# Kernel tuning notes

Hardware: AMD Instinct MI355X
Metric: run time of the kernel (lower is better)

## Reference

```python
import jax, jax.numpy as jnp
import numpy as np

B, S, D = 4, 2048, 1152
H, KVH, HD = 16, 4, 64
SW = 1792
NEG = jnp.float32(-1e9)


def setup_inputs() -> dict:
    key = jax.random.key(0)
    ks = jax.random.split(key, 6)
    x = jax.random.normal(ks[0], (B, S, D), jnp.float32)
    s = 0.02
    wq = jax.random.normal(ks[1], (H * HD, D), jnp.float32) * s
    wk = jax.random.normal(ks[2], (KVH * HD, D), jnp.float32) * s
    wv = jax.random.normal(ks[3], (KVH * HD, D), jnp.float32) * s
    wo = jax.random.normal(ks[4], (D, H * HD), jnp.float32) * s
    # rotary freqs: theta=10000, standard llama-style
    inv = 1.0 / (10000.0 ** (np.arange(0, HD, 2, dtype=np.float32) / HD))
    t = np.arange(S, dtype=np.float32)
    fr = np.outer(t, inv)  # [S, HD//2]
    freqs_cos = jnp.asarray(np.cos(fr), jnp.float32)
    freqs_sin = jnp.asarray(np.sin(fr), jnp.float32)
    positions = jnp.arange(S, dtype=jnp.int32)
    # sliding-window causal additive mask: attend j iff 0 <= i-j < SW
    i = jnp.arange(S)[:, None]
    j = jnp.arange(S)[None, :]
    allowed = (j <= i) & (i - j < SW)
    mask = jnp.where(allowed, jnp.float32(0.0), NEG)
    cache_k = jnp.zeros((B, SW, KVH, HD), jnp.float32)
    cache_v = jnp.zeros((B, SW, KVH, HD), jnp.float32)
    return {"x": x, "wq": wq, "wk": wk, "wv": wv, "wo": wo,
            "freqs_cos": freqs_cos, "freqs_sin": freqs_sin, "mask": mask,
            "cache_k": cache_k, "cache_v": cache_v, "positions": positions}


def _rope(t, cos, sin):
    # t: [B,S,h,HD]; complex multiply on (even, odd) pairs
    tr = t.reshape(t.shape[:-1] + (HD // 2, 2))
    a, b = tr[..., 0], tr[..., 1]
    c = cos[None, :, None, :]
    s = sin[None, :, None, :]
    out = jnp.stack([a * c - b * s, a * s + b * c], axis=-1)
    return out.reshape(t.shape)


def reference(x, wq, wk, wv, wo, freqs_cos, freqs_sin, mask, cache_k, cache_v, positions):
    bsz, seqlen, _ = x.shape
    xq = jnp.einsum('bsd,ed->bse', x, wq).reshape(bsz, seqlen, H, HD)
    xk = jnp.einsum('bsd,ed->bse', x, wk).reshape(bsz, seqlen, KVH, HD)
    xv = jnp.einsum('bsd,ed->bse', x, wv).reshape(bsz, seqlen, KVH, HD)
    xq = _rope(xq, freqs_cos, freqs_sin)
    xk = _rope(xk, freqs_cos, freqs_sin)
    # circular-buffer cache scatter (last SW tokens, modulo indexing)
    idx = positions[-SW:] % SW
    new_ck = cache_k.at[:, idx].set(xk[:, -SW:])
    new_cv = cache_v.at[:, idx].set(xv[:, -SW:])
    # GQA: expand kv heads (repeat_interleave on head dim)
    rep = H // KVH
    key = jnp.repeat(xk, rep, axis=2)   # [B,S,H,HD]
    value = jnp.repeat(xv, rep, axis=2)
    q = xq.transpose(0, 2, 1, 3)        # [B,H,S,HD]
    k = key.transpose(0, 2, 1, 3)
    v = value.transpose(0, 2, 1, 3)
    scale = 1.0 / jnp.sqrt(jnp.float32(HD))
    scores = jnp.einsum('bhqd,bhkd->bhqk', q, k) * scale + mask[None, None]
    probs = jax.nn.softmax(scores, axis=-1)
    out = jnp.einsum('bhqk,bhkd->bhqd', probs, v)
    out = out.transpose(0, 2, 1, 3).reshape(bsz, seqlen, H * HD)
    out = jnp.einsum('bse,de->bsd', out, wo)
    return out, new_ck, new_cv
```

## Files before the change

kernel.cpp:

```cpp
#include <hip/hip_runtime.h>
#include <cstdint>
#include <cstddef>


typedef unsigned short u16;
typedef unsigned int   u32;
typedef __attribute__((ext_vector_type(8))) short bf16x8;
typedef __attribute__((ext_vector_type(4))) float f32x4;

#define AS1(p) ((const __attribute__((address_space(1))) void*)(p))
#define AS3(p) ((__attribute__((address_space(3))) void*)(p))

__device__ __forceinline__ u16 f2bf(float f) {
  u32 u = __float_as_uint(f);
  u += 0x7fffu + ((u >> 16) & 1u);
  return (u16)(u >> 16);
}
__device__ __forceinline__ float bf2f(u32 x) { return __uint_as_float(x << 16); }
__device__ __forceinline__ f32x4 mfma16(bf16x8 a, bf16x8 b, f32x4 c) {
  return __builtin_amdgcn_mfma_f32_16x16x32_bf16(a, b, c, 0, 0, 0);
}
__device__ __forceinline__ u32 cvtpk_bf16(float lo, float hi) {
  u32 r;
  asm("v_cvt_pk_bf16_f32 %0, %1, %2" : "=v"(r) : "v"(lo), "v"(hi));
  return r;
}

__global__ __launch_bounds__(256) void cvt4_kernel(const float* __restrict__ wq,
                                                   const float* __restrict__ wk,
                                                   const float* __restrict__ wv,
                                                   const float* __restrict__ wo,
                                                   u16* __restrict__ wqkvb,
                                                   u16* __restrict__ wob) {
  int i = blockIdx.x * 256 + threadIdx.x;
  const float* in; u16* out; int off;
  if (i < 294912)       { in = wq; out = wqkvb;               off = i; }
  else if (i < 368640)  { in = wk; out = wqkvb + 1024 * 1152; off = i - 294912; }
  else if (i < 442368)  { in = wv; out = wqkvb + 1280 * 1152; off = i - 368640; }
  else                  { in = wo; out = wob;                 off = i - 442368; }
  float4 v = ((const float4*)in)[off];
  uint2 o;
  o.x = (u32)f2bf(v.x) | ((u32)f2bf(v.y) << 16);
  o.y = (u32)f2bf(v.z) | ((u32)f2bf(v.w) << 16);
  ((uint2*)out)[off] = o;
}

template<int BF16_OUT, int A_FP32>
__global__ __launch_bounds__(256) void gemm_bt(const void* __restrict__ Araw,
                                               const u16* __restrict__ B,
                                               void* __restrict__ C,
                                               int M, int N, int K, int NT) {
  __shared__ u16 As[128][64];
  __shared__ u16 Bs[128][64];
  const int tid  = threadIdx.x;
  const int w    = tid >> 6, lane = tid & 63;
  const int l15  = lane & 15, hi4 = lane >> 4;
  const int lid  = blockIdx.x;
  const int k_   = lid >> 3;
  const int by   = (lid & 7) + 8 * (k_ / NT);
  const int bx   = k_ % NT;
  const int m0   = by * 128, n0 = bx * 128;
  const int wr   = w >> 1, wc = w & 1;

  const int srow = lane >> 3;
  const int slot = lane & 7;
  const int scol = (slot ^ srow) << 3;
  const u16*   Ab  = (const u16*)Araw + (size_t)(m0 + w * 32 + srow) * K + scol;
  const float* Af  = (const float*)Araw + (size_t)(m0 + w * 32 + srow) * K + slot * 8;
  const u16*   Bb  = B + (size_t)(n0 + w * 32 + srow) * K + scol;
  u16* AsDst = &As[w * 32][0];
  u16* BsDst = &Bs[w * 32][0];

  const int swz = (l15 & 7) << 4;
  const int c0  = (((hi4 * 16)      ^ swz) >> 1);
  const int c1  = (((64 + hi4 * 16) ^ swz) >> 1);
  const u16* aRd = &As[wr * 64 + l15][0];
  const u16* bRd = &Bs[wc * 64 + l15][0];

  f32x4 acc[4][4] = {};

  for (int kk = 0; kk < K; kk += 64) {
#pragma unroll
    for (int q = 0; q < 4; q++) {
      if (A_FP32) {
        const float* src = Af + kk + (size_t)q * 8 * K;
        float4 f0 = *(const float4*)src;
        float4 f1 = *(const float4*)(src + 4);
        u32 d[4];
        d[0] = cvtpk_bf16(f0.x, f0.y);
        d[1] = cvtpk_bf16(f0.z, f0.w);
        d[2] = cvtpk_bf16(f1.x, f1.y);
        d[3] = cvtpk_bf16(f1.z, f1.w);
        *(uint4*)&As[w * 32 + q * 8 + srow][scol] = *(uint4*)&d[0];
      } else {
        __builtin_amdgcn_global_load_lds(AS1(Ab + kk + (size_t)q * 8 * K),
                                         AS3(AsDst + q * 8 * 64), 16, 0, 0);
      }
      __builtin_amdgcn_global_load_lds(AS1(Bb + kk + (size_t)q * 8 * K),
                                       AS3(BsDst + q * 8 * 64), 16, 0, 0);
    }
    __syncthreads();
#pragma unroll
    for (int ks = 0; ks < 2; ks++) {
      const int cc = ks ? c1 : c0;
      bf16x8 af[4], bfr[4];
#pragma unroll
      for (int t = 0; t < 4; t++) af[t]  = *(const bf16x8*)(aRd + t * 16 * 64 + cc);
#pragma unroll
      for (int t = 0; t < 4; t++) bfr[t] = *(const bf16x8*)(bRd + t * 16 * 64 + cc);
#pragma unroll
      for (int mi = 0; mi < 4; mi++)
#pragma unroll
        for (int ni = 0; ni < 4; ni++)
          acc[mi][ni] = mfma16(af[mi], bfr[ni], acc[mi][ni]);
    }
    __syncthreads();
  }

#pragma unroll
  for (int mi = 0; mi < 4; mi++) {
#pragma unroll
    for (int r = 0; r < 4; r++) {
      int row = m0 + wr * 64 + mi * 16 + hi4 * 4 + r;
      size_t base = (size_t)row * N + n0 + wc * 64 + l15;
#pragma unroll
      for (int ni = 0; ni < 4; ni++) {
        float v = acc[mi][ni][r];
        if (BF16_OUT) ((u16*)C)[base + ni * 16] = f2bf(v);
        else          ((float*)C)[base + ni * 16] = v;
      }
    }
  }
}

__global__ __launch_bounds__(256) void ropev_kernel(u16* __restrict__ buf,
                                                    float* __restrict__ kcache,
                                                    u16* __restrict__ vT,
                                                    float* __restrict__ ncv,
                                                    const float* __restrict__ cosT,
                                                    const float* __restrict__ sinT) {
  __shared__ u16 tile[64][65];
  if (blockIdx.x < 4096) {
    int idx = blockIdx.x * 256 + threadIdx.x;
    int m = idx >> 7, p = idx & 127;
    int s = m & 2047, b = m >> 11;
    int hh = p & 31;
    u32* bp = (u32*)buf + (size_t)m * 768 + 512 + p;
    u32 pk = *bp;
    float a  = bf2f(pk & 0xffffu), bb = bf2f(pk >> 16);
    float c  = cosT[s * 32 + hh],  sn = sinT[s * 32 + hh];
    float o0 = a * c - bb * sn;
    float o1 = a * sn + bb * c;
    *bp = (u32)f2bf(o0) | ((u32)f2bf(o1) << 16);
    if (s >= 256) {
      int pc = (s < 1792) ? s : s - 1792;
      float2* cp = (float2*)(kcache + (size_t)(b * 1792 + pc) * 256 + 2 * p);
      *cp = make_float2(o0, o1);
    }
  } else {
    int bi = blockIdx.x - 4096;
    int s0 = (bi & 31) * 64, kvh = (bi >> 5) & 3, b = bi >> 7;
    int t = threadIdx.x;
    int r = t >> 2, cc = (t & 3) * 16;
    const u16* src = buf + (size_t)(b * 2048 + s0 + r) * 1536 + 1280 + kvh * 64 + cc;
    uint4 v0 = *(const uint4*)src;
    uint4 v1 = *(const uint4*)(src + 8);
    u16 vals[16];
    *(uint4*)&vals[0] = v0;
    *(uint4*)&vals[8] = v1;
    int s = s0 + r;
    if (s >= 256) {
      int pc = (s < 1792) ? s : s - 1792;
      float* dst = ncv + (size_t)(b * 1792 + pc) * 256 + kvh * 64 + cc;
#pragma unroll
      for (int i = 0; i < 16; i += 4) {
        float4 f = make_float4(bf2f(vals[i]), bf2f(vals[i + 1]),
                               bf2f(vals[i + 2]), bf2f(vals[i + 3]));
        *(float4*)(dst + i) = f;
      }
    }
#pragma unroll
    for (int i = 0; i < 16; i++) tile[cc + i][r] = vals[i];
    __syncthreads();
    u16 ov[16];
#pragma unroll
    for (int i = 0; i < 16; i++) {
      int p = cc + i;
      int pg = p & 31, e = pg & 7, g = pg >> 3;
      int key = (p & ~31) + ((e < 4) ? (4 * g + e) : (16 + 4 * g + (e - 4)));
      ov[i] = tile[r][key];
    }
    u16* dst2 = vT + (size_t)((b * 4 + kvh) * 64 + r) * 2048 + s0 + cc;
    *(uint4*)dst2 = *(uint4*)&ov[0];
    *(uint4*)(dst2 + 8) = *(uint4*)&ov[8];
  }
}

__global__ __launch_bounds__(256) void attn_kernel(const u16* __restrict__ qkv,
                                                   const u16* __restrict__ vT,
                                                   u16* __restrict__ attnb,
                                                   const float* __restrict__ cosT,
                                                   const float* __restrict__ sinT) {
  __shared__ __align__(16) u16 Kbuf[2][64][64];
  __shared__ __align__(16) u16 Vbuf[2][64][64];
  const int tid = threadIdx.x;
  const int w = tid >> 6, lane = tid & 63;
  const int l15 = lane & 15, hi4 = lane >> 4;

  const int lid  = blockIdx.x;
  const int wgid = (lid & 7) * 128 + (lid >> 3);
  const int gx   = wgid & 63;
  const int rr   = wgid >> 6;
  const int kvh  = rr & 3, b = rr >> 2;
  const int i0   = 32 * (63 - gx);
  const int h    = kvh * 4 + w;

  const u16* qbase = qkv + (size_t)(b * 2048) * 1536 + h * 64;
  const u16* kbase = qkv + (size_t)(b * 2048) * 1536 + 1024 + kvh * 64;
  const u16* vbase = vT + (size_t)((b * 4 + kvh) * 64) * 2048;

  const float qs = 0.18033688011112042f;
  bf16x8 qa[2][2];
  {
    const u16* qp = qbase + (size_t)(i0 + l15) * 1536 + hi4 * 8;
#pragma unroll
    for (int m = 0; m < 2; m++) {
      const int s = i0 + m * 16 + l15;
#pragma unroll
      for (int ki = 0; ki < 2; ki++) {
        bf16x8 qv = *(const bf16x8*)(qp + m * 16 * 1536 + ki * 32);
        const int hh0 = ki * 16 + hi4 * 4;
        float4 cs = *(const float4*)(cosT + s * 32 + hh0);
        float4 sn = *(const float4*)(sinT + s * 32 + hh0);
        cs.x *= qs; cs.y *= qs; cs.z *= qs; cs.w *= qs;
        sn.x *= qs; sn.y *= qs; sn.z *= qs; sn.w *= qs;
        u32 wds[4];
        {
          float a = bf2f((u16)qv[0]), bb2 = bf2f((u16)qv[1]);
          wds[0] = cvtpk_bf16(a * cs.x - bb2 * sn.x, a * sn.x + bb2 * cs.x);
        }
        {
          float a = bf2f((u16)qv[2]), bb2 = bf2f((u16)qv[3]);
          wds[1] = cvtpk_bf16(a * cs.y - bb2 * sn.y, a * sn.y + bb2 * cs.y);
        }
        {
          float a = bf2f((u16)qv[4]), bb2 = bf2f((u16)qv[5]);
          wds[2] = cvtpk_bf16(a * cs.z - bb2 * sn.z, a * sn.z + bb2 * cs.z);
        }
        {
          float a = bf2f((u16)qv[6]), bb2 = bf2f((u16)qv[7]);
          wds[3] = cvtpk_bf16(a * cs.w - bb2 * sn.w, a * sn.w + bb2 * cs.w);
        }
        qa[m][ki] = *(const bf16x8*)&wds[0];
      }
    }
  }

  bf16x8 ones;
#pragma unroll
  for (int i = 0; i < 8; i++) ones[i] = (short)0x3F80;

  f32x4 o[2][4] = {};
  f32x4 ol[2] = {};

  const int srow = lane >> 3;
  const int ssl  = (lane & 7) ^ srow;

#define STAGE(J0, BS)                                                                     \
  do {                                                                                    \
    _Pragma("unroll")                                                                     \
    for (int q = 0; q < 2; q++) {                                                         \
      const int row = 32 * q + 8 * w + srow;                                              \
      __builtin_amdgcn_global_load_lds(AS1(kbase + (size_t)((J0) + row) * 1536 + ssl * 8),\
                                       AS3(&Kbuf[BS][32 * q + 8 * w][0]), 16, 0, 0);      \
      __builtin_amdgcn_global_load_lds(AS1(vbase + (size_t)row * 2048 + (J0) + ssl * 8),  \
                                       AS3(&Vbuf[BS][32 * q + 8 * w][0]), 16, 0, 0);      \
    }                                                                                     \
  } while (0)

  int jstart = i0 - 1791;
  if (jstart < 0) jstart = 0;
  jstart &= ~63;
  const int jend = i0 + 32;
  const int ntiles = (jend - jstart + 63) >> 6;

  STAGE(jstart, 0);
  if (ntiles > 1) STAGE(jstart + 64, 1);

  for (int t = 0; t < ntiles; t++) {
    const int j0 = jstart + 64 * t;
    if (t + 1 < ntiles) asm volatile("s_waitcnt vmcnt(4)" ::: "memory");
    else                asm volatile("s_waitcnt vmcnt(0)" ::: "memory");
    __builtin_amdgcn_s_barrier();
    __builtin_amdgcn_sched_barrier(0);

    const u16* Kb = &Kbuf[t & 1][0][0];
    const u16* Vb = &Vbuf[t & 1][0][0];

    bf16x8 kf[2][4];
#pragma unroll
    for (int nt = 0; nt < 4; nt++)
#pragma unroll
      for (int ki = 0; ki < 2; ki++)
        kf[ki][nt] = *(const bf16x8*)(Kb + (nt * 16 + l15) * 64 +
                                      (((ki * 4 + hi4) ^ (l15 & 7)) << 3));

    bf16x8 vf[2][4];
#pragma unroll
    for (int tt = 0; tt < 4; tt++) {
      const int row = tt * 16 + l15;
#pragma unroll
      for (int kbp = 0; kbp < 2; kbp++)
        vf[kbp][tt] = *(const bf16x8*)(Vb + row * 64 +
                                       (((kbp * 4 + hi4) ^ (l15 & 7)) << 3));
    }

    __builtin_amdgcn_s_setprio(1);
    const bool fast = (j0 + 63 <= i0) && (i0 + 31 - j0 < 1792);
#pragma unroll
    for (int m = 0; m < 2; m++) {
      __align__(16) u32 pkb[8];
#pragma unroll
      for (int nt = 0; nt < 4; nt++) {
        f32x4 s = {0.f, 0.f, 0.f, 0.f};
        s = mfma16(kf[0][nt], qa[m][0], s);
        s = mfma16(kf[1][nt], qa[m][1], s);
        float p[4];
        if (fast) {
#pragma unroll
          for (int r = 0; r < 4; r++) p[r] = __builtin_amdgcn_exp2f(s[r]);
        } else {
          const int i = i0 + m * 16 + l15;
#pragma unroll
          for (int r = 0; r < 4; r++) {
            const int j = j0 + nt * 16 + hi4 * 4 + r;
            p[r] = (j <= i && i - j < 1792) ? __builtin_amdgcn_exp2f(s[r]) : 0.f;
          }
        }
        pkb[nt * 2]     = cvtpk_bf16(p[0], p[1]);
        pkb[nt * 2 + 1] = cvtpk_bf16(p[2], p[3]);
      }
      bf16x8 pa0 = *(const bf16x8*)&pkb[0];
      bf16x8 pa1 = *(const bf16x8*)&pkb[4];
#pragma unroll
      for (int tt = 0; tt < 4; tt++) {
        o[m][tt] = mfma16(pa0, vf[0][tt], o[m][tt]);
        o[m][tt] = mfma16(pa1, vf[1][tt], o[m][tt]);
      }
      ol[m] = mfma16(pa0, ones, ol[m]);
      ol[m] = mfma16(pa1, ones, ol[m]);
    }
    __builtin_amdgcn_s_setprio(0);

    __builtin_amdgcn_s_barrier();
    __builtin_amdgcn_sched_barrier(0);
    if (t + 2 < ntiles) STAGE(j0 + 128, t & 1);
  }
#undef STAGE

  u16* op = attnb + (size_t)(b * 2048 + i0 + hi4 * 4) * 1024 + h * 64 + l15;
#pragma unroll
  for (int m = 0; m < 2; m++)
#pragma unroll
    for (int r = 0; r < 4; r++) {
      float inv = 1.0f / ol[m][r];
#pragma unroll
      for (int tt = 0; tt < 4; tt++)
        op[(size_t)(m * 16 + r) * 1024 + 16 * tt] = f2bf(o[m][tt][r] * inv);
    }
}

extern "C" void kernel_launch(void* const* d_in, const int* in_sizes, int n_in,
                              void* d_out, int out_size, void* d_ws, size_t ws_size,
                              hipStream_t stream) {
  const float* x  = (const float*)d_in[0];
  const float* wq = (const float*)d_in[1];
  const float* wk = (const float*)d_in[2];
  const float* wv = (const float*)d_in[3];
  const float* wo = (const float*)d_in[4];
  const float* fc = (const float*)d_in[5];
  const float* fs = (const float*)d_in[6];

  float* out = (float*)d_out;
  float* nck = out + 9437184;
  float* ncv = nck + 1835008;

  char* ws = (char*)d_ws;
  u16* attnb = (u16*)(ws);
  u16* wqkvb = (u16*)(ws + 18874368);
  u16* wob   = (u16*)(ws + 22413312);
  u16* qkv   = (u16*)(ws + 24772608);
  u16* vT    = (u16*)(ws + 49938432);

  cvt4_kernel<<<2880, 256, 0, stream>>>(wq, wk, wv, wo, wqkvb, wob);

  gemm_bt<1, 1><<<768, 256, 0, stream>>>(x, wqkvb, qkv, 8192, 1536, 1152, 12);

  ropev_kernel<<<4608, 256, 0, stream>>>(qkv, nck, vT, ncv, fc, fs);

  attn_kernel<<<1024, 256, 0, stream>>>(qkv, vT, attnb, fc, fs);

  gemm_bt<0, 0><<<576, 256, 0, stream>>>(attnb, wob, out, 8192, 1152, 1024, 9);
}
```

Measured before the change: 152.0 us.

## Prefetch fp32 A tiles in QKV GEMM and move wo conversion into rope kernel

After: 149.7 us (median of 2 runs). About the same (-1.5%).

```diff
diff --git a/kernel.cpp b/kernel.cpp
--- a/kernel.cpp
+++ b/kernel.cpp
@@ -26,18 +26,15 @@
   return r;
 }
 
-__global__ __launch_bounds__(256) void cvt4_kernel(const float* __restrict__ wq,
+__global__ __launch_bounds__(256) void cvt3_kernel(const float* __restrict__ wq,
                                                    const float* __restrict__ wk,
                                                    const float* __restrict__ wv,
-                                                   const float* __restrict__ wo,
-                                                   u16* __restrict__ wqkvb,
-                                                   u16* __restrict__ wob) {
+                                                   u16* __restrict__ wqkvb) {
   int i = blockIdx.x * 256 + threadIdx.x;
   const float* in; u16* out; int off;
   if (i < 294912)       { in = wq; out = wqkvb;               off = i; }
   else if (i < 368640)  { in = wk; out = wqkvb + 1024 * 1152; off = i - 294912; }
-  else if (i < 442368)  { in = wv; out = wqkvb + 1280 * 1152; off = i - 368640; }
-  else                  { in = wo; out = wob;                 off = i - 442368; }
+  else                  { in = wv; out = wqkvb + 1280 * 1152; off = i - 368640; }
   float4 v = ((const float4*)in)[off];
   uint2 o;
   o.x = (u32)f2bf(v.x) | ((u32)f2bf(v.y) << 16);
@@ -79,42 +76,83 @@
 
   f32x4 acc[4][4] = {};
 
-  for (int kk = 0; kk < K; kk += 64) {
+  if (A_FP32) {
+    float4 pfa[4][2];
 #pragma unroll
     for (int q = 0; q < 4; q++) {
-      if (A_FP32) {
-        const float* src = Af + kk + (size_t)q * 8 * K;
-        float4 f0 = *(const float4*)src;
-        float4 f1 = *(const float4*)(src + 4);
+      const float* src = Af + (size_t)q * 8 * K;
+      pfa[q][0] = *(const float4*)src;
+      pfa[q][1] = *(const float4*)(src + 4);
+    }
+    for (int kk = 0; kk < K; kk += 64) {
+#pragma unroll
+      for (int q = 0; q < 4; q++) {
+        __builtin_amdgcn_global_load_lds(AS1(Bb + kk + (size_t)q * 8 * K),
+                                         AS3(BsDst + q * 8 * 64), 16, 0, 0);
         u32 d[4];
-        d[0] = cvtpk_bf16(f0.x, f0.y);
-        d[1] = cvtpk_bf16(f0.z, f0.w);
-        d[2] = cvtpk_bf16(f1.x, f1.y);
-        d[3] = cvtpk_bf16(f1.z, f1.w);
+        d[0] = cvtpk_bf16(pfa[q][0].x, pfa[q][0].y);
+        d[1] = cvtpk_bf16(pfa[q][0].z, pfa[q][0].w);
+        d[2] = cvtpk_bf16(pfa[q][1].x, pfa[q][1].y);
+        d[3] = cvtpk_bf16(pfa[q][1].z, pfa[q][1].w);
         *(uint4*)&As[w * 32 + q * 8 + srow][scol] = *(uint4*)&d[0];
-      } else {
+      }
+      __builtin_amdgcn_sched_barrier(0);
+      if (kk + 64 < K) {
+#pragma unroll
+        for (int q = 0; q < 4; q++) {
+          const float* src = Af + kk + 64 + (size_t)q * 8 * K;
+          pfa[q][0] = *(const float4*)src;
+          pfa[q][1] = *(const float4*)(src + 4);
+        }
+      }
+      __builtin_amdgcn_sched_barrier(0);
+      if (kk + 64 < K) asm volatile("s_waitcnt vmcnt(8) lgkmcnt(0)" ::: "memory");
+      else             asm volatile("s_waitcnt vmcnt(0) lgkmcnt(0)" ::: "memory");
+      __builtin_amdgcn_s_barrier();
+      __builtin_amdgcn_sched_barrier(0);
+#pragma unroll
+      for (int ks = 0; ks < 2; ks++) {
+        const int cc = ks ? c1 : c0;
+        bf16x8 af[4], bfr[4];
+#pragma unroll
+        for (int t = 0; t < 4; t++) af[t]  = *(const bf16x8*)(aRd + t * 16 * 64 + cc);
+#pragma unroll
+        for (int t = 0; t < 4; t++) bfr[t] = *(const bf16x8*)(bRd + t * 16 * 64 + cc);
+#pragma unroll
+        for (int mi = 0; mi < 4; mi++)
+#pragma unroll
+          for (int ni = 0; ni < 4; ni++)
+            acc[mi][ni] = mfma16(af[mi], bfr[ni], acc[mi][ni]);
+      }
+      __builtin_amdgcn_s_barrier();
+      __builtin_amdgcn_sched_barrier(0);
+    }
+  } else {
+    for (int kk = 0; kk < K; kk += 64) {
+#pragma unroll
+      for (int q = 0; q < 4; q++) {
         __builtin_amdgcn_global_load_lds(AS1(Ab + kk + (size_t)q * 8 * K),
                                          AS3(AsDst + q * 8 * 64), 16, 0, 0);
-      }
-      __builtin_amdgcn_global_load_lds(AS1(Bb + kk + (size_t)q * 8 * K),
-                                       AS3(BsDst + q * 8 * 64), 16, 0, 0);
-    }
-    __syncthreads();
-#pragma unroll
-    for (int ks = 0; ks < 2; ks++) {
-      const int cc = ks ? c1 : c0;
-      bf16x8 af[4], bfr[4];
-#pragma unroll
-      for (int t = 0; t < 4; t++) af[t]  = *(const bf16x8*)(aRd + t * 16 * 64 + cc);
-#pragma unroll
-      for (int t = 0; t < 4; t++) bfr[t] = *(const bf16x8*)(bRd + t * 16 * 64 + cc);
-#pragma unroll
-      for (int mi = 0; mi < 4; mi++)
-#pragma unroll
-        for (int ni = 0; ni < 4; ni++)
-          acc[mi][ni] = mfma16(af[mi], bfr[ni], acc[mi][ni]);
-    }
-    __syncthreads();
+        __builtin_amdgcn_global_load_lds(AS1(Bb + kk + (size_t)q * 8 * K),
+                                         AS3(BsDst + q * 8 * 64), 16, 0, 0);
+      }
+      __syncthreads();
+#pragma unroll
+      for (int ks = 0; ks < 2; ks++) {
+        const int cc = ks ? c1 : c0;
+        bf16x8 af[4], bfr[4];
+#pragma unroll
+        for (int t = 0; t < 4; t++) af[t]  = *(const bf16x8*)(aRd + t * 16 * 64 + cc);
+#pragma unroll
+        for (int t = 0; t < 4; t++) bfr[t] = *(const bf16x8*)(bRd + t * 16 * 64 + cc);
+#pragma unroll
+        for (int mi = 0; mi < 4; mi++)
+#pragma unroll
+          for (int ni = 0; ni < 4; ni++)
+            acc[mi][ni] = mfma16(af[mi], bfr[ni], acc[mi][ni]);
+      }
+      __syncthreads();
+    }
   }
 
 #pragma unroll
@@ -137,6 +175,8 @@
                                                     float* __restrict__ kcache,
                                                     u16* __restrict__ vT,
                                                     float* __restrict__ ncv,
+                                                    const float* __restrict__ wo,
+                                                    u16* __restrict__ wob,
                                                     const float* __restrict__ cosT,
                                                     const float* __restrict__ sinT) {
   __shared__ u16 tile[64][65];
@@ -157,7 +197,7 @@
       float2* cp = (float2*)(kcache + (size_t)(b * 1792 + pc) * 256 + 2 * p);
       *cp = make_float2(o0, o1);
     }
-  } else {
+  } else if (blockIdx.x < 4608) {
     int bi = blockIdx.x - 4096;
     int s0 = (bi & 31) * 64, kvh = (bi >> 5) & 3, b = bi >> 7;
     int t = threadIdx.x;
@@ -193,6 +233,13 @@
     u16* dst2 = vT + (size_t)((b * 4 + kvh) * 64 + r) * 2048 + s0 + cc;
     *(uint4*)dst2 = *(uint4*)&ov[0];
     *(uint4*)(dst2 + 8) = *(uint4*)&ov[8];
+  } else {
+    int i = (blockIdx.x - 4608) * 256 + threadIdx.x;
+    float4 v = ((const float4*)wo)[i];
+    uint2 o;
+    o.x = (u32)f2bf(v.x) | ((u32)f2bf(v.y) << 16);
+    o.y = (u32)f2bf(v.z) | ((u32)f2bf(v.w) << 16);
+    ((uint2*)wob)[i] = o;
   }
 }
 
@@ -392,11 +439,11 @@
   u16* qkv   = (u16*)(ws + 24772608);
   u16* vT    = (u16*)(ws + 49938432);
 
-  cvt4_kernel<<<2880, 256, 0, stream>>>(wq, wk, wv, wo, wqkvb, wob);
+  cvt3_kernel<<<1728, 256, 0, stream>>>(wq, wk, wv, wqkvb);
 
   gemm_bt<1, 1><<<768, 256, 0, stream>>>(x, wqkvb, qkv, 8192, 1536, 1152, 12);
 
-  ropev_kernel<<<4608, 256, 0, stream>>>(qkv, nck, vT, ncv, fc, fs);
+  ropev_kernel<<<5760, 256, 0, stream>>>(qkv, nck, vT, ncv, wo, wob, fc, fs);
 
   attn_kernel<<<1024, 256, 0, stream>>>(qkv, vT, attnb, fc, fs);
 
```
